# Optimization experiments

Measured on AMD Instinct MI355X. Metric: run time of the kernel, lower is better.

The kernel has to match this reference:

```python
import jax, jax.numpy as jnp
import numpy as np

B, N, H = 4, 256, 256
BN_EPS = 1e-5
ETA_EPS = 1e-20


def setup_inputs() -> dict:
    key = jax.random.key(0)
    k1, k2, k3, k4 = jax.random.split(key, 4)
    scale = 1.0 / np.sqrt(H)
    return {
        "nodes_features": jax.random.normal(k1, (B, N, H), dtype=jnp.float32),
        "edges_features": jax.random.normal(k2, (B, N, N, H), dtype=jnp.float32),
        "W1": jax.random.normal(k3, (H, H), dtype=jnp.float32) * scale,
        "W2": jax.random.normal(k4, (H, H), dtype=jnp.float32) * scale,
        "gamma": jnp.ones((H,), dtype=jnp.float32),
        "beta": jnp.zeros((H,), dtype=jnp.float32),
    }


def reference(nodes_features, edges_features, W1, W2, gamma, beta):
    # Linear projections (nn.Linear: y = x @ W.T, no bias)
    x_left = jnp.einsum('bnh,oh->bno', nodes_features, W1)       # (B,N,H)
    x_w2 = jnp.einsum('bnh,oh->bno', nodes_features, W2)         # (B,N,H)

    # Edge gating: sigmoid-normalize over neighbor axis j (dim=2)
    sig = jax.nn.sigmoid(edges_features)                         # (B,N,N,H)
    eta = sig / (jnp.sum(sig, axis=2, keepdims=True) + ETA_EPS)  # (B,N,N,H)

    # Weighted aggregation: sum_j eta[b,i,j,h] * x_w2[b,j,h]
    right = jnp.einsum('bijh,bjh->bih', eta, x_w2)               # (B,N,H)

    equ = x_left + right                                         # (B,N,H)

    # BatchNorm1d over channel H with batch stats over (B, N) (training mode,
    # track_running_stats=False -> always uses batch statistics, biased var)
    mean = jnp.mean(equ, axis=(0, 1))                            # (H,)
    var = jnp.var(equ, axis=(0, 1))                              # (H,) biased
    normed = (equ - mean) * jax.lax.rsqrt(var + BN_EPS)
    return normed * gamma + beta
```

## Files before the change

kernel.cpp:

```cpp
#include <hip/hip_runtime.h>
#include <cstddef>

#define BB 4
#define NN 256
#define HH 256
#define BN_EPS 1e-5f
#define ETA_EPS 1e-20f

typedef float f4 __attribute__((ext_vector_type(4)));

__device__ __forceinline__ float fast_sigmoid(float x) {
    float ex = __expf(-x);
    return __builtin_amdgcn_rcpf(1.f + ex);
}

__global__ __launch_bounds__(256) void transpose_kernel(
    const float* __restrict__ W1, const float* __restrict__ W2,
    float* __restrict__ WT1, float* __restrict__ WT2)
{
    const int which = blockIdx.x >> 4;
    const int tile  = blockIdx.x & 15;
    const int tr = (tile >> 2) << 6, tc = (tile & 3) << 6;
    const float* __restrict__ W  = which ? W2 : W1;
    float* __restrict__ WT       = which ? WT2 : WT1;

    __shared__ float tl[64][65];
    const int c = threadIdx.x & 63, p0 = threadIdx.x >> 6;
#pragma unroll
    for (int p = 0; p < 16; ++p) {
        int r = p * 4 + p0;
        tl[c][r] = W[(tr + r) * HH + tc + c];
    }
    __syncthreads();
#pragma unroll
    for (int p = 0; p < 16; ++p) {
        int cc = p * 4 + p0;
        WT[(tc + cc) * HH + tr + c] = tl[cc][c];
    }
}

__global__ __launch_bounds__(256) void proj_kernel(
    const float* __restrict__ nodes, const float* __restrict__ WT1,
    const float* __restrict__ WT2, float* __restrict__ xleft,
    float* __restrict__ xw2)
{
    const int which = blockIdx.x >> 7;
    const int rb    = blockIdx.x & 127;
    const float* __restrict__ WT = which ? WT2 : WT1;
    float* __restrict__ out      = which ? xw2 : xleft;
    const int t = threadIdx.x;

    __shared__ float xs[8][HH];
    {
        f4* xs4 = reinterpret_cast<f4*>(xs);
        const f4* nodes4 = reinterpret_cast<const f4*>(nodes) + rb * 512;
#pragma unroll
        for (int m = 0; m < 2; ++m) xs4[m * 256 + t] = nodes4[m * 256 + t];
    }
    __syncthreads();

    const int oq = t & 63;
    const int hg = t >> 6;
    const f4* __restrict__ WT4 = reinterpret_cast<const f4*>(WT);

    f4 acc[8];
#pragma unroll
    for (int r = 0; r < 8; ++r) acc[r] = (f4){0.f, 0.f, 0.f, 0.f};

    for (int hh = 0; hh < 64; ++hh) {
        const int h = hg * 64 + hh;
        f4 wv = WT4[h * 64 + oq];
#pragma unroll
        for (int r = 0; r < 8; ++r)
            acc[r] += xs[r][h] * wv;
    }

    __shared__ f4 ps[4][8][64];
#pragma unroll
    for (int r = 0; r < 8; ++r) ps[hg][r][oq] = acc[r];
    __syncthreads();

#pragma unroll
    for (int m = 0; m < 2; ++m) {
        int idx = m * 256 + t;
        int r = idx >> 6, o = idx & 63;
        f4 v = ps[0][r][o] + ps[1][r][o] + ps[2][r][o] + ps[3][r][o];
        reinterpret_cast<f4*>(out)[(rb * 8 + r) * 64 + o] = v;
    }
}

__global__ __launch_bounds__(1024) void edge_kernel(
    const float* __restrict__ edges, const float* __restrict__ xw2,
    const float* __restrict__ xleft, float* __restrict__ equ)
{
    const int blk = blockIdx.x;
    const int ig  = blk >> 2;
    const int hs4 = (blk & 3) * 16;
    const int bi0 = ig * 8;
    const int b   = bi0 >> 8;
    const int t   = threadIdx.x;

    __shared__ f4 xw_s[NN][16];

    const f4* __restrict__ xw4 =
        reinterpret_cast<const f4*>(xw2) + (size_t)b * NN * 64;
#pragma unroll
    for (int m = 0; m < 4; ++m) {
        int idx = m * 1024 + t;
        int j = idx >> 4, q = idx & 15;
        xw_s[j][q] = xw4[j * 64 + hs4 + q];
    }
    __syncthreads();

    const int q  = t & 15;
    const int il = (t >> 4) & 7;
    const int jg = t >> 7;

    const f4* __restrict__ erow =
        reinterpret_cast<const f4*>(edges) +
        (size_t)(bi0 + il) * (NN * 64) + hs4 + q;

    float s0[4] = {0.f, 0.f, 0.f, 0.f};
    float s1[4] = {0.f, 0.f, 0.f, 0.f};

#pragma unroll 2
    for (int j = jg; j < NN; j += 8) {
        f4 e  = __builtin_nontemporal_load(erow + j * 64);
        f4 xw = xw_s[j][q];
#pragma unroll
        for (int k = 0; k < 4; ++k) {
            float sg = fast_sigmoid(e[k]);
            s0[k] += sg;
            s1[k] += sg * xw[k];
        }
    }
    __syncthreads();

    float* red = reinterpret_cast<float*>(xw_s);
    {
        float* r0 = red + ((jg * 8 + il) * 16 + q) * 4;
        float* r1 = r0 + 4096;
#pragma unroll
        for (int k = 0; k < 4; ++k) { r0[k] = s0[k]; r1[k] = s1[k]; }
    }
    __syncthreads();

    if (t < 512) {
        const int il2 = t >> 6;
        const int ch  = t & 63;
        float S0 = 0.f, S1 = 0.f;
#pragma unroll
        for (int g = 0; g < 8; ++g) {
            S0 += red[(g * 8 + il2) * 64 + ch];
            S1 += red[(g * 8 + il2) * 64 + ch + 4096];
        }
        const size_t off = (size_t)(bi0 + il2) * HH + hs4 * 4 + ch;
        equ[off] = xleft[off] + S1 / (S0 + ETA_EPS);
    }
}

__global__ __launch_bounds__(1024) void statsnorm_kernel(
    const float* __restrict__ equ, const float* __restrict__ gamma,
    const float* __restrict__ beta, float* __restrict__ out)
{
    const int cq = blockIdx.x;
    const int t  = threadIdx.x;
    const int lane = t & 63, w = t >> 6;

    f4 v = reinterpret_cast<const f4*>(equ)[t * 64 + cq];
    f4 s = v;
    f4 qs = v * v;

#pragma unroll
    for (int off = 32; off >= 1; off >>= 1) {
#pragma unroll
        for (int k = 0; k < 4; ++k) {
            s[k]  += __shfl_xor(s[k], off);
            qs[k] += __shfl_xor(qs[k], off);
        }
    }

    __shared__ f4 ws_[16][2];
    if (lane == 0) { ws_[w][0] = s; ws_[w][1] = qs; }
    __syncthreads();

    __shared__ f4 sc_s, sh_s;
    if (t == 0) {
        f4 S = (f4){0.f, 0.f, 0.f, 0.f};
        f4 Q = (f4){0.f, 0.f, 0.f, 0.f};
#pragma unroll
        for (int g = 0; g < 16; ++g) { S += ws_[g][0]; Q += ws_[g][1]; }
        const float inv_n = 1.f / (float)(BB * NN);
        f4 gm = reinterpret_cast<const f4*>(gamma)[cq];
        f4 bt = reinterpret_cast<const f4*>(beta)[cq];
        f4 sc, sh;
#pragma unroll
        for (int k = 0; k < 4; ++k) {
            float mean = S[k] * inv_n;
            float var  = Q[k] * inv_n - mean * mean;
            float rstd = rsqrtf(var + BN_EPS);
            sc[k] = rstd * gm[k];
            sh[k] = bt[k] - mean * rstd * gm[k];
        }
        sc_s = sc; sh_s = sh;
    }
    __syncthreads();

    f4 sc = sc_s, sh = sh_s;
    f4 o;
#pragma unroll
    for (int k = 0; k < 4; ++k) o[k] = v[k] * sc[k] + sh[k];
    reinterpret_cast<f4*>(out)[t * 64 + cq] = o;
}

extern "C" void kernel_launch(void* const* d_in, const int* in_sizes, int n_in,
                              void* d_out, int out_size, void* d_ws, size_t ws_size,
                              hipStream_t stream) {
    (void)in_sizes; (void)n_in; (void)out_size; (void)ws_size;

    const float* nodes = (const float*)d_in[0];
    const float* edges = (const float*)d_in[1];
    const float* W1    = (const float*)d_in[2];
    const float* W2    = (const float*)d_in[3];
    const float* gamma = (const float*)d_in[4];
    const float* beta  = (const float*)d_in[5];
    float* out = (float*)d_out;

    const int nBN_H = BB * NN * HH;
    float* ws    = (float*)d_ws;
    float* xleft = ws;
    float* xw2   = ws + nBN_H;
    float* equ   = ws + 2 * nBN_H;
    float* WT1   = ws + 3 * nBN_H;
    float* WT2   = WT1 + HH * HH;

    transpose_kernel<<<32, 256, 0, stream>>>(W1, W2, WT1, WT2);
    proj_kernel<<<256, 256, 0, stream>>>(nodes, WT1, WT2, xleft, xw2);
    edge_kernel<<<512, 1024, 0, stream>>>(edges, xw2, xleft, equ);
    statsnorm_kernel<<<64, 1024, 0, stream>>>(equ, gamma, beta, out);
}
```

Before: 73.98 us.

## Fuse BatchNorm statistics into edge kernel via atomics; simplify norm kernel

Each edge_kernel block now reduces the sum and sum of squares of its equ outputs per channel in shared memory and adds them atomically into global accumulators, which the transpose launch zeroes. The separate stats+normalize kernel becomes a simple elementwise norm kernel over 256 blocks instead of 64 blocks of 1024 threads. The edge load also drops its nontemporal hint. This removes a block-level reduction pass from the tail, at the cost of atomic contention and nondeterministic summation order.

New measurement: 65.67 us. 1.13x faster.

```diff
diff --git a/kernel.cpp b/kernel.cpp
--- a/kernel.cpp
+++ b/kernel.cpp
@@ -16,8 +16,14 @@
 
 __global__ __launch_bounds__(256) void transpose_kernel(
     const float* __restrict__ W1, const float* __restrict__ W2,
-    float* __restrict__ WT1, float* __restrict__ WT2)
-{
+    float* __restrict__ WT1, float* __restrict__ WT2,
+    float* __restrict__ Ssum, float* __restrict__ Qsum)
+{
+    if (blockIdx.x == 32) {
+        Ssum[threadIdx.x] = 0.f;
+        Qsum[threadIdx.x] = 0.f;
+        return;
+    }
     const int which = blockIdx.x >> 4;
     const int tile  = blockIdx.x & 15;
     const int tr = (tile >> 2) << 6, tc = (tile & 3) << 6;
@@ -91,7 +97,8 @@
 
 __global__ __launch_bounds__(1024) void edge_kernel(
     const float* __restrict__ edges, const float* __restrict__ xw2,
-    const float* __restrict__ xleft, float* __restrict__ equ)
+    const float* __restrict__ xleft, float* __restrict__ equ,
+    float* __restrict__ Ssum, float* __restrict__ Qsum)
 {
     const int blk = blockIdx.x;
     const int ig  = blk >> 2;
@@ -125,7 +132,7 @@
 
 #pragma unroll 2
     for (int j = jg; j < NN; j += 8) {
-        f4 e  = __builtin_nontemporal_load(erow + j * 64);
+        f4 e  = erow[j * 64];
         f4 xw = xw_s[j][q];
 #pragma unroll
         for (int k = 0; k < 4; ++k) {
@@ -145,6 +152,8 @@
     }
     __syncthreads();
 
+    float* st = red + 8192;
+
     if (t < 512) {
         const int il2 = t >> 6;
         const int ch  = t & 63;
@@ -155,62 +164,48 @@
             S1 += red[(g * 8 + il2) * 64 + ch + 4096];
         }
         const size_t off = (size_t)(bi0 + il2) * HH + hs4 * 4 + ch;
-        equ[off] = xleft[off] + S1 / (S0 + ETA_EPS);
-    }
-}
-
-__global__ __launch_bounds__(1024) void statsnorm_kernel(
-    const float* __restrict__ equ, const float* __restrict__ gamma,
+        float ov = xleft[off] + S1 / (S0 + ETA_EPS);
+        equ[off] = ov;
+        st[(il2 * 64 + ch) * 2]     = ov;
+        st[(il2 * 64 + ch) * 2 + 1] = ov * ov;
+    }
+    __syncthreads();
+
+    if (t < 64) {
+        float S = 0.f, Q = 0.f;
+#pragma unroll
+        for (int g = 0; g < 8; ++g) {
+            S += st[(g * 64 + t) * 2];
+            Q += st[(g * 64 + t) * 2 + 1];
+        }
+        atomicAdd(&Ssum[hs4 * 4 + t], S);
+        atomicAdd(&Qsum[hs4 * 4 + t], Q);
+    }
+}
+
+__global__ __launch_bounds__(256) void norm_kernel(
+    const float* __restrict__ equ, const float* __restrict__ Ssum,
+    const float* __restrict__ Qsum, const float* __restrict__ gamma,
     const float* __restrict__ beta, float* __restrict__ out)
 {
-    const int cq = blockIdx.x;
-    const int t  = threadIdx.x;
-    const int lane = t & 63, w = t >> 6;
-
-    f4 v = reinterpret_cast<const f4*>(equ)[t * 64 + cq];
-    f4 s = v;
-    f4 qs = v * v;
-
-#pragma unroll
-    for (int off = 32; off >= 1; off >>= 1) {
-#pragma unroll
-        for (int k = 0; k < 4; ++k) {
-            s[k]  += __shfl_xor(s[k], off);
-            qs[k] += __shfl_xor(qs[k], off);
-        }
-    }
-
-    __shared__ f4 ws_[16][2];
-    if (lane == 0) { ws_[w][0] = s; ws_[w][1] = qs; }
-    __syncthreads();
-
-    __shared__ f4 sc_s, sh_s;
-    if (t == 0) {
-        f4 S = (f4){0.f, 0.f, 0.f, 0.f};
-        f4 Q = (f4){0.f, 0.f, 0.f, 0.f};
-#pragma unroll
-        for (int g = 0; g < 16; ++g) { S += ws_[g][0]; Q += ws_[g][1]; }
-        const float inv_n = 1.f / (float)(BB * NN);
-        f4 gm = reinterpret_cast<const f4*>(gamma)[cq];
-        f4 bt = reinterpret_cast<const f4*>(beta)[cq];
-        f4 sc, sh;
-#pragma unroll
-        for (int k = 0; k < 4; ++k) {
-            float mean = S[k] * inv_n;
-            float var  = Q[k] * inv_n - mean * mean;
-            float rstd = rsqrtf(var + BN_EPS);
-            sc[k] = rstd * gm[k];
-            sh[k] = bt[k] - mean * rstd * gm[k];
-        }
-        sc_s = sc; sh_s = sh;
-    }
-    __syncthreads();
-
-    f4 sc = sc_s, sh = sh_s;
+    const int idx = blockIdx.x * 256 + threadIdx.x;
+    const int c4  = idx & 63;
+    f4 e = reinterpret_cast<const f4*>(equ)[idx];
+    f4 S = reinterpret_cast<const f4*>(Ssum)[c4];
+    f4 Q = reinterpret_cast<const f4*>(Qsum)[c4];
+    f4 g = reinterpret_cast<const f4*>(gamma)[c4];
+    f4 b = reinterpret_cast<const f4*>(beta)[c4];
+
+    const float inv_n = 1.f / (float)(BB * NN);
     f4 o;
 #pragma unroll
-    for (int k = 0; k < 4; ++k) o[k] = v[k] * sc[k] + sh[k];
-    reinterpret_cast<f4*>(out)[t * 64 + cq] = o;
+    for (int k = 0; k < 4; ++k) {
+        float mean = S[k] * inv_n;
+        float var  = Q[k] * inv_n - mean * mean;
+        float rstd = rsqrtf(var + BN_EPS);
+        o[k] = (e[k] - mean) * rstd * g[k] + b[k];
+    }
+    reinterpret_cast<f4*>(out)[idx] = o;
 }
 
 extern "C" void kernel_launch(void* const* d_in, const int* in_sizes, int n_in,
@@ -233,9 +228,11 @@
     float* equ   = ws + 2 * nBN_H;
     float* WT1   = ws + 3 * nBN_H;
     float* WT2   = WT1 + HH * HH;
-
-    transpose_kernel<<<32, 256, 0, stream>>>(W1, W2, WT1, WT2);
+    float* Ssum  = WT2 + HH * HH;
+    float* Qsum  = Ssum + HH;
+
+    transpose_kernel<<<33, 256, 0, stream>>>(W1, W2, WT1, WT2, Ssum, Qsum);
     proj_kernel<<<256, 256, 0, stream>>>(nodes, WT1, WT2, xleft, xw2);
-    edge_kernel<<<512, 1024, 0, stream>>>(edges, xw2, xleft, equ);
-    statsnorm_kernel<<<64, 1024, 0, stream>>>(equ, gamma, beta, out);
-}
+    edge_kernel<<<512, 1024, 0, stream>>>(edges, xw2, xleft, equ, Ssum, Qsum);
+    norm_kernel<<<256, 256, 0, stream>>>(equ, Ssum, Qsum, gamma, beta, out);
+}
```
